# Kernel optimization log

Measured on AMD Instinct MI355X. Metric: run time of the kernel, lower is better.

The kernel has to match this reference:

```python
import jax, jax.numpy as jnp
import numpy as np

HD = 64        # hidden_dim
H = 4          # heads
N = 50000      # nodes
E = 400000     # edges (before self loops)
NEG_ATT = 0.2  # GATConv attention LeakyReLU slope (PyG default)
NEG_ACT = 0.01 # nn.LeakyReLU() default slope
EPS = 1e-5     # BatchNorm eps


def _bn(x, gamma, beta):
    # training-mode BatchNorm1d over node dimension (biased variance)
    mu = x.mean(0)
    var = x.var(0)
    return gamma * (x - mu) * jax.lax.rsqrt(var + EPS) + beta


def _gatconv(h_in, src, dst, W, a_src, a_dst, bias, heads, outc, concat):
    n = h_in.shape[0]
    h = (h_in @ W.T).reshape(n, heads, outc)              # [N,H,C]
    al_s = jnp.einsum('nhc,hc->nh', h, a_src)             # [N,H]
    al_d = jnp.einsum('nhc,hc->nh', h, a_dst)
    e = jax.nn.leaky_relu(al_s[src] + al_d[dst], NEG_ATT) # [E',H]
    # softmax over incoming edges of each destination node
    m = jax.lax.stop_gradient(jax.ops.segment_max(e, dst, num_segments=n))
    ex = jnp.exp(e - m[dst])
    den = jax.ops.segment_sum(ex, dst, num_segments=n)
    alpha = ex / den[dst]                                  # [E',H]
    out = jax.ops.segment_sum(h[src] * alpha[..., None], dst, num_segments=n)
    out = out.reshape(n, heads * outc) if concat else out.mean(axis=1)
    return out + bias


def setup_inputs() -> dict:
    ks = jax.random.split(jax.random.key(0), 20)
    s = 0.1
    d = {
        'x': jax.random.normal(ks[0], (N, 2 * HD), jnp.float32),
        'edge_index': jax.random.randint(ks[1], (2, E), 0, N, jnp.int64),
        'W1': jax.random.normal(ks[2], (H * HD, 2 * HD), jnp.float32) * s,
        'a1s': jax.random.normal(ks[3], (H, HD), jnp.float32) * s,
        'a1d': jax.random.normal(ks[4], (H, HD), jnp.float32) * s,
        'b1': jnp.zeros((H * HD,), jnp.float32),
        'W2': jax.random.normal(ks[5], (H * HD, H * HD), jnp.float32) * s,
        'a2s': jax.random.normal(ks[6], (H, HD), jnp.float32) * s,
        'a2d': jax.random.normal(ks[7], (H, HD), jnp.float32) * s,
        'b2': jnp.zeros((H * HD,), jnp.float32),
        'W3': jax.random.normal(ks[8], (1 * HD, H * HD), jnp.float32) * s,
        'a3s': jax.random.normal(ks[9], (1, HD), jnp.float32) * s,
        'a3d': jax.random.normal(ks[10], (1, HD), jnp.float32) * s,
        'b3': jnp.zeros((HD,), jnp.float32),
        'gamma': jnp.ones((H * HD,), jnp.float32),
        'beta': jnp.zeros((H * HD,), jnp.float32),
    }
    return d


def reference(x, edge_index, W1, a1s, a1d, b1, W2, a2s, a2d, b2,
              W3, a3s, a3d, b3, gamma, beta):
    n = x.shape[0]
    loop = jnp.arange(n, dtype=edge_index.dtype)
    src = jnp.concatenate([edge_index[0], loop])  # add_self_loops=True
    dst = jnp.concatenate([edge_index[1], loop])

    h = _gatconv(x, src, dst, W1, a1s, a1d, b1, H, HD, True)
    h = jax.nn.leaky_relu(_bn(h, gamma, beta), NEG_ACT)

    # single middle residual block (num_layers=3); dropout is identity (eval)
    res = h
    h = _gatconv(h, src, dst, W2, a2s, a2d, b2, H, HD, True)
    h = jax.nn.leaky_relu(_bn(h, gamma, beta), NEG_ACT)
    h = h + res

    out = _gatconv(h, src, dst, W3, a3s, a3d, b3, 1, HD, False)
    return out
```

## Files before the change

kernel.cpp:

```cpp
#include <hip/hip_runtime.h>
#include <hip/hip_bf16.h>

#define NEG_ATT 0.2f
#define NEG_ACT 0.01f

typedef __attribute__((ext_vector_type(8))) short short8;
typedef __attribute__((ext_vector_type(4))) float f32x4;

__device__ __forceinline__ unsigned short f2bf(float f) {
    unsigned int u = __float_as_uint(f);
    unsigned int r = (u + 0x7fff + ((u >> 16) & 1)) >> 16;
    return (unsigned short)r;
}
__device__ __forceinline__ float b2f(unsigned short h) {
    return __uint_as_float((unsigned int)h << 16);
}


__global__ void count_edges(const int* __restrict__ ei, int* deg, int E) {
    int t = blockIdx.x * 256 + threadIdx.x;
    if (t < E) atomicAdd(&deg[ei[E + t]], 1);
}

#define SCAN_CHUNK 1024
__global__ void scan1(const int* __restrict__ deg, int* __restrict__ offs,
                      int* blocksum, int Nn) {
    __shared__ int sh[256];
    int b = blockIdx.x, t = threadIdx.x;
    int base = b * SCAN_CHUNK + t * 4;
    int v[4];
    int s = 0;
    for (int j = 0; j < 4; j++) {
        int idx = base + j;
        v[j] = (idx < Nn) ? deg[idx] : 0;
        s += v[j];
    }
    sh[t] = s;
    __syncthreads();
    for (int off = 1; off < 256; off <<= 1) {
        int x = (t >= off) ? sh[t - off] : 0;
        __syncthreads();
        sh[t] += x;
        __syncthreads();
    }
    int excl = sh[t] - s;
    if (t == 255) blocksum[b] = sh[255];
    int run = excl;
    for (int j = 0; j < 4; j++) {
        int idx = base + j;
        if (idx < Nn) offs[idx] = run;
        run += v[j];
    }
}

__global__ void scan23(int* __restrict__ offs, const int* __restrict__ bsum,
                       int* __restrict__ cursor, int Nn, int G) {
    int i = blockIdx.x * 256 + threadIdx.x;
    if (i > Nn) return;
    int g = i >> 10;
    int basev = 0;
    for (int k = 0; k < g; k++) basev += bsum[k];
    if (i == Nn) {
        int tot = basev;
        for (int k = g; k < G; k++) tot += bsum[k];
        offs[Nn] = tot;
        return;
    }
    int v = offs[i] + basev;
    offs[i] = v;
    cursor[i] = v;
}

__global__ void fill_csr(const int* __restrict__ ei, int* cursor, int* csr, int E, int Nn) {
    int t = blockIdx.x * 256 + threadIdx.x;
    if (t < E) {
        int s = ei[t];
        int d = ei[E + t];
        int p = atomicAdd(&cursor[d], 1);
        csr[p] = s;
    } else if (t < E + Nn) {
        int nn = t - E;
        int p = atomicAdd(&cursor[nn], 1);
        csr[p] = nn;
    }
}


__global__ __launch_bounds__(256) void prep_all(
    int* __restrict__ deg, int Nn,
    const float* __restrict__ x, unsigned short* __restrict__ xb, int nx, int nxpad,
    const float* __restrict__ w1, unsigned short* __restrict__ o1, int n1,
    const float* __restrict__ w2, unsigned short* __restrict__ o2, int n2,
    const float* __restrict__ w3, unsigned short* __restrict__ o3, int n3) {
    int id = blockIdx.x * 256 + threadIdx.x;
    int nconv = (nxpad + n1 + n2 + n3) / 8;
    if (id >= nconv) {
        int d0 = (id - nconv) * 8;
        for (int k = 0; k < 8; k++)
            if (d0 + k < Nn) deg[d0 + k] = 1;
        return;
    }
    int i = id * 8;
    const float* in;
    unsigned short* out;
    if (i < nxpad) {
        if (i >= nx) {
            *(ushort4*)&xb[i] = make_ushort4(0, 0, 0, 0);
            *(ushort4*)&xb[i + 4] = make_ushort4(0, 0, 0, 0);
            return;
        }
        in = x + i; out = xb + i;
    } else {
        int j = i - nxpad;
        if (j < n1) { in = w1 + j; out = o1 + j; }
        else if (j < n1 + n2) { in = w2 + (j - n1); out = o2 + (j - n1); }
        else { in = w3 + (j - n1 - n2); out = o3 + (j - n1 - n2); }
    }
    float4 a = *(const float4*)in;
    float4 b = *(const float4*)(in + 4);
    *(ushort4*)out = make_ushort4(f2bf(a.x), f2bf(a.y), f2bf(a.z), f2bf(a.w));
    *(ushort4*)(out + 4) = make_ushort4(f2bf(b.x), f2bf(b.y), f2bf(b.z), f2bf(b.w));
}


template <int K, int CO, int HEADS>
__global__ __launch_bounds__(256) void gemm_mfma(
    const unsigned short* __restrict__ Xb, const unsigned short* __restrict__ Wb,
    unsigned short* __restrict__ Hb, const float* __restrict__ a_s,
    const float* __restrict__ a_d, float* __restrict__ als, float* __restrict__ ald) {
    constexpr int BM = 128, BN = 64, BK = 64, LD = 72, SLD = 68;
    __shared__ __align__(16) char smem[4 * 32 * SLD * 4];
    unsigned short* As = (unsigned short*)smem;
    unsigned short* Bs = As + BM * LD;
    int tid = threadIdx.x;
    int wave = tid >> 6, lane = tid & 63;
    int quad = lane >> 4, l16 = lane & 15;
    int m0 = blockIdx.x * BM, n0 = blockIdx.y * BN;
    int hd = blockIdx.y;
    int arow = tid >> 3;
    int achk = (tid & 7) * 8;
    f32x4 acc[2][4] = {};
    for (int k0 = 0; k0 < K; k0 += BK) {
        __syncthreads();
#pragma unroll
        for (int p = 0; p < 4; p++) {
            int r = arow + p * 32;
            *(int4*)&As[r * LD + achk] = *(const int4*)&Xb[(size_t)(m0 + r) * K + k0 + achk];
        }
#pragma unroll
        for (int p = 0; p < 2; p++) {
            int r = arow + p * 32;
            *(int4*)&Bs[r * LD + achk] = *(const int4*)&Wb[(size_t)(n0 + r) * K + k0 + achk];
        }
        __syncthreads();
#pragma unroll
        for (int ks = 0; ks < 2; ks++) {
            short8 af[2], bfr[4];
#pragma unroll
            for (int i = 0; i < 2; i++)
                af[i] = *(const short8*)&As[(wave * 32 + i * 16 + l16) * LD + ks * 32 + quad * 8];
#pragma unroll
            for (int j = 0; j < 4; j++)
                bfr[j] = *(const short8*)&Bs[(j * 16 + l16) * LD + ks * 32 + quad * 8];
#pragma unroll
            for (int i = 0; i < 2; i++)
#pragma unroll
                for (int j = 0; j < 4; j++)
                    acc[i][j] = __builtin_amdgcn_mfma_f32_16x16x32_bf16(af[i], bfr[j], acc[i][j], 0, 0, 0);
        }
    }
    __syncthreads();

    float asv[4], adv[4];
#pragma unroll
    for (int j = 0; j < 4; j++) {
        asv[j] = a_s[hd * 64 + j * 16 + l16];
        adv[j] = a_d[hd * 64 + j * 16 + l16];
    }
#pragma unroll
    for (int i = 0; i < 2; i++)
#pragma unroll
        for (int r = 0; r < 4; r++) {
            float ps = acc[i][0][r] * asv[0] + acc[i][1][r] * asv[1] +
                       acc[i][2][r] * asv[2] + acc[i][3][r] * asv[3];
            float pd = acc[i][0][r] * adv[0] + acc[i][1][r] * adv[1] +
                       acc[i][2][r] * adv[2] + acc[i][3][r] * adv[3];
#pragma unroll
            for (int mm = 1; mm < 16; mm <<= 1) {
                ps += __shfl_xor(ps, mm);
                pd += __shfl_xor(pd, mm);
            }
            if (l16 == 0) {
                int m = m0 + wave * 32 + i * 16 + quad * 4 + r;
                als[m * HEADS + hd] = ps;
                ald[m * HEADS + hd] = pd;
            }
        }

    float* stg = (float*)smem + wave * 32 * SLD;
#pragma unroll
    for (int i = 0; i < 2; i++)
#pragma unroll
        for (int j = 0; j < 4; j++)
#pragma unroll
            for (int r = 0; r < 4; r++)
                stg[(i * 16 + quad * 4 + r) * SLD + j * 16 + l16] = acc[i][j][r];
    int g = lane >> 3, c8 = (lane & 7) * 8;
#pragma unroll
    for (int p = 0; p < 4; p++) {
        int row = p * 8 + g;
        float4 v0 = *(const float4*)&stg[row * SLD + c8];
        float4 v1 = *(const float4*)&stg[row * SLD + c8 + 4];
        uint4 o;
        o.x = ((unsigned)f2bf(v0.y) << 16) | f2bf(v0.x);
        o.y = ((unsigned)f2bf(v0.w) << 16) | f2bf(v0.z);
        o.z = ((unsigned)f2bf(v1.y) << 16) | f2bf(v1.x);
        o.w = ((unsigned)f2bf(v1.w) << 16) | f2bf(v1.z);
        *(uint4*)&Hb[(size_t)(m0 + wave * 32 + row) * CO + n0 + c8] = o;
    }
}


#define EDGE4(sA, sB, sC, sD)                                                        \
    {                                                                                \
        float a0 = als[(sA)*4 + hd], a1 = als[(sB)*4 + hd];                          \
        float a2 = als[(sC)*4 + hd], a3 = als[(sD)*4 + hd];                          \
        ushort4 h0 = *(const ushort4*)&Hb[(size_t)(sA)*256 + c4];                    \
        ushort4 h1 = *(const ushort4*)&Hb[(size_t)(sB)*256 + c4];                    \
        ushort4 h2 = *(const ushort4*)&Hb[(size_t)(sC)*256 + c4];                    \
        ushort4 h3 = *(const ushort4*)&Hb[(size_t)(sD)*256 + c4];                    \
        float e0 = a0 + aldn; e0 = e0 > 0.f ? e0 : NEG_ATT * e0;                     \
        float e1 = a1 + aldn; e1 = e1 > 0.f ? e1 : NEG_ATT * e1;                     \
        float e2 = a2 + aldn; e2 = e2 > 0.f ? e2 : NEG_ATT * e2;                     \
        float e3 = a3 + aldn; e3 = e3 > 0.f ? e3 : NEG_ATT * e3;                     \
        float w0 = __expf(e0), w1 = __expf(e1), w2 = __expf(e2), w3 = __expf(e3);    \
        den += (w0 + w1) + (w2 + w3);                                                \
        acc.x += w0 * b2f(h0.x) + w1 * b2f(h1.x) + w2 * b2f(h2.x) + w3 * b2f(h3.x);  \
        acc.y += w0 * b2f(h0.y) + w1 * b2f(h1.y) + w2 * b2f(h2.y) + w3 * b2f(h3.y);  \
        acc.z += w0 * b2f(h0.z) + w1 * b2f(h1.z) + w2 * b2f(h2.z) + w3 * b2f(h3.z);  \
        acc.w += w0 * b2f(h0.w) + w1 * b2f(h1.w) + w2 * b2f(h2.w) + w3 * b2f(h3.w);  \
    }

__global__ __launch_bounds__(256) void aggregate_h4(
    const unsigned short* __restrict__ Hb, const float* __restrict__ als,
    const float* __restrict__ ald, const int* __restrict__ offs,
    const int* __restrict__ csr, unsigned short* __restrict__ Yb, int Nn) {
    int wave = threadIdx.x >> 6;
    int lane = threadIdx.x & 63;
    int n = blockIdx.x * 4 + wave;
    if (n >= Nn) return;
    int hd = lane >> 4;
    int c4 = lane * 4;
    float aldn = ald[n * 4 + hd];
    int beg = offs[n], end = offs[n + 1];
    float4 acc = make_float4(0.f, 0.f, 0.f, 0.f);
    float den = 0.f;
    for (int b = beg; b < end; b += 64) {
        int cnt = min(64, end - b);
        int idx = 0;
        if (lane < cnt) idx = csr[b + lane];
        int j = 0;
        for (; j + 8 <= cnt; j += 8) {
            int s0 = __shfl(idx, j), s1 = __shfl(idx, j + 1);
            int s2 = __shfl(idx, j + 2), s3 = __shfl(idx, j + 3);
            int s4 = __shfl(idx, j + 4), s5 = __shfl(idx, j + 5);
            int s6 = __shfl(idx, j + 6), s7 = __shfl(idx, j + 7);
            EDGE4(s0, s1, s2, s3);
            EDGE4(s4, s5, s6, s7);
        }
        for (; j + 4 <= cnt; j += 4) {
            int s0 = __shfl(idx, j), s1 = __shfl(idx, j + 1);
            int s2 = __shfl(idx, j + 2), s3 = __shfl(idx, j + 3);
            EDGE4(s0, s1, s2, s3);
        }
        for (; j < cnt; j++) {
            int s = __shfl(idx, j);
            float e = als[s * 4 + hd] + aldn;
            e = e > 0.f ? e : NEG_ATT * e;
            float w = __expf(e);
            den += w;
            ushort4 hv = *(const ushort4*)&Hb[(size_t)s * 256 + c4];
            acc.x += w * b2f(hv.x); acc.y += w * b2f(hv.y);
            acc.z += w * b2f(hv.z); acc.w += w * b2f(hv.w);
        }
    }
    float inv = 1.f / den;
    *(ushort4*)&Yb[(size_t)n * 256 + c4] = make_ushort4(
        f2bf(acc.x * inv), f2bf(acc.y * inv), f2bf(acc.z * inv), f2bf(acc.w * inv));
}

__global__ __launch_bounds__(256) void aggregate_h1(
    const unsigned short* __restrict__ Hb, const float* __restrict__ als,
    const float* __restrict__ ald, const int* __restrict__ offs,
    const int* __restrict__ csr, const float* __restrict__ bias,
    float* __restrict__ Yout, int Nn) {
    int wave = threadIdx.x >> 6;
    int lane = threadIdx.x & 63;
    int sub = lane >> 4, lane16 = lane & 15;
    int n = blockIdx.x * 16 + wave * 4 + sub;
    if (n >= Nn) return;
    int c4 = lane16 * 4;
    float aldn = ald[n];
    int beg = offs[n], end = offs[n + 1];
    float4 acc = make_float4(0.f, 0.f, 0.f, 0.f);
    float den = 0.f;
    for (int b = beg; b < end; b += 16) {
        int cnt = min(16, end - b);
        int idx = 0;
        if (lane16 < cnt) idx = csr[b + lane16];
        int j = 0;
        for (; j + 4 <= cnt; j += 4) {
            int s0 = __shfl(idx, (sub << 4) + j);
            int s1 = __shfl(idx, (sub << 4) + j + 1);
            int s2 = __shfl(idx, (sub << 4) + j + 2);
            int s3 = __shfl(idx, (sub << 4) + j + 3);
            float a0 = als[s0], a1 = als[s1], a2 = als[s2], a3 = als[s3];
            ushort4 h0 = *(const ushort4*)&Hb[(size_t)s0 * 64 + c4];
            ushort4 h1 = *(const ushort4*)&Hb[(size_t)s1 * 64 + c4];
            ushort4 h2 = *(const ushort4*)&Hb[(size_t)s2 * 64 + c4];
            ushort4 h3 = *(const ushort4*)&Hb[(size_t)s3 * 64 + c4];
            float e0 = a0 + aldn; e0 = e0 > 0.f ? e0 : NEG_ATT * e0;
            float e1 = a1 + aldn; e1 = e1 > 0.f ? e1 : NEG_ATT * e1;
            float e2 = a2 + aldn; e2 = e2 > 0.f ? e2 : NEG_ATT * e2;
            float e3 = a3 + aldn; e3 = e3 > 0.f ? e3 : NEG_ATT * e3;
            float w0 = __expf(e0), w1 = __expf(e1), w2 = __expf(e2), w3 = __expf(e3);
            den += (w0 + w1) + (w2 + w3);
            acc.x += w0 * b2f(h0.x) + w1 * b2f(h1.x) + w2 * b2f(h2.x) + w3 * b2f(h3.x);
            acc.y += w0 * b2f(h0.y) + w1 * b2f(h1.y) + w2 * b2f(h2.y) + w3 * b2f(h3.y);
            acc.z += w0 * b2f(h0.z) + w1 * b2f(h1.z) + w2 * b2f(h2.z) + w3 * b2f(h3.z);
            acc.w += w0 * b2f(h0.w) + w1 * b2f(h1.w) + w2 * b2f(h2.w) + w3 * b2f(h3.w);
        }
        for (; j < cnt; j++) {
            int s = __shfl(idx, (sub << 4) + j);
            float e = als[s] + aldn;
            e = e > 0.f ? e : NEG_ATT * e;
            float w = __expf(e);
            den += w;
            ushort4 hv = *(const ushort4*)&Hb[(size_t)s * 64 + c4];
            acc.x += w * b2f(hv.x); acc.y += w * b2f(hv.y);
            acc.z += w * b2f(hv.z); acc.w += w * b2f(hv.w);
        }
    }
    float inv = 1.f / den;
    float4 bv = *(const float4*)&bias[c4];
    float4 o = make_float4(acc.x * inv + bv.x, acc.y * inv + bv.y,
                           acc.z * inv + bv.z, acc.w * inv + bv.w);
    *(float4*)&Yout[(size_t)n * 64 + c4] = o;
}


__global__ __launch_bounds__(256) void bn_stats(const unsigned short* __restrict__ Yb,
                                                float* __restrict__ partial, int Nn) {
    __shared__ float red[4 * 512];
    int t = threadIdx.x;
    int g = blockIdx.x;
    int rows_per = (Nn + gridDim.x - 1) / gridDim.x;
    int r0 = g * rows_per;
    int r1 = min(r0 + rows_per, Nn);
    int sub = t >> 6;
    int c4 = (t & 63) * 4;
    float4 s = make_float4(0.f, 0.f, 0.f, 0.f);
    float4 q = make_float4(0.f, 0.f, 0.f, 0.f);
    for (int r = r0 + sub; r < r1; r += 4) {
        ushort4 u = *(const ushort4*)&Yb[(size_t)r * 256 + c4];
        float vx = b2f(u.x), vy = b2f(u.y), vz = b2f(u.z), vw = b2f(u.w);
        s.x += vx; s.y += vy; s.z += vz; s.w += vw;
        q.x += vx * vx; q.y += vy * vy; q.z += vz * vz; q.w += vw * vw;
    }
    float* rs = &red[sub * 512];
    rs[c4 + 0] = s.x; rs[c4 + 1] = s.y; rs[c4 + 2] = s.z; rs[c4 + 3] = s.w;
    rs[256 + c4 + 0] = q.x; rs[256 + c4 + 1] = q.y;
    rs[256 + c4 + 2] = q.z; rs[256 + c4 + 3] = q.w;
    __syncthreads();
    float v0 = red[t] + red[512 + t] + red[1024 + t] + red[1536 + t];
    float v1 = red[256 + t] + red[768 + t] + red[1280 + t] + red[1792 + t];
    partial[(size_t)g * 512 + t] = v0;
    partial[(size_t)g * 512 + 256 + t] = v1;
}

__global__ __launch_bounds__(256) void bn_reduce_final(
    const float* __restrict__ partial, int NP, const float* __restrict__ gamma,
    const float* __restrict__ beta, float* scale, float* shift, int Nn) {
    __shared__ float sh[8];
    int ch = blockIdx.x;
    int t = threadIdx.x;
    int wave = t >> 6, lane = t & 63;
    float s = 0.f, q = 0.f;
    for (int i = t; i < NP; i += 256) {
        s += partial[(size_t)i * 512 + ch];
        q += partial[(size_t)i * 512 + 256 + ch];
    }
    for (int off = 32; off; off >>= 1) {
        s += __shfl_down(s, off);
        q += __shfl_down(q, off);
    }
    if (lane == 0) { sh[wave] = s; sh[4 + wave] = q; }
    __syncthreads();
    if (t == 0) {
        s = sh[0] + sh[1] + sh[2] + sh[3];
        q = sh[4] + sh[5] + sh[6] + sh[7];
        float inv_n = 1.f / (float)Nn;
        float mu = s * inv_n;
        float var = q * inv_n - mu * mu;
        float sc = gamma[ch] * rsqrtf(var + 1e-5f);
        scale[ch] = sc;
        shift[ch] = beta[ch] - mu * sc;
    }
}

template <bool RES>
__global__ __launch_bounds__(256) void bn_apply(const unsigned short* __restrict__ Yb,
                                                const float* __restrict__ scale,
                                                const float* __restrict__ shift,
                                                unsigned short* __restrict__ OutB,
                                                int total4, int total4pad) {
    int i = blockIdx.x * 256 + threadIdx.x;
    if (i >= total4pad) return;
    if (i >= total4) {
        *(ushort4*)&OutB[i * 4] = make_ushort4(0, 0, 0, 0);
        return;
    }
    ushort4 u = *(const ushort4*)&Yb[i * 4];
    int cb = (i * 4) & 255;
    float4 sc = *(const float4*)&scale[cb];
    float4 sh = *(const float4*)&shift[cb];
    float4 o;
    o.x = sc.x * b2f(u.x) + sh.x; o.x = o.x > 0.f ? o.x : NEG_ACT * o.x;
    o.y = sc.y * b2f(u.y) + sh.y; o.y = o.y > 0.f ? o.y : NEG_ACT * o.y;
    o.z = sc.z * b2f(u.z) + sh.z; o.z = o.z > 0.f ? o.z : NEG_ACT * o.z;
    o.w = sc.w * b2f(u.w) + sh.w; o.w = o.w > 0.f ? o.w : NEG_ACT * o.w;
    if (RES) {
        ushort4 r = *(const ushort4*)&OutB[i * 4];
        o.x += b2f(r.x); o.y += b2f(r.y); o.z += b2f(r.z); o.w += b2f(r.w);
    }
    *(ushort4*)&OutB[i * 4] = make_ushort4(f2bf(o.x), f2bf(o.y), f2bf(o.z), f2bf(o.w));
}


extern "C" void kernel_launch(void* const* d_in, const int* in_sizes, int n_in,
                              void* d_out, int out_size, void* d_ws, size_t ws_size,
                              hipStream_t stream) {
    const float* x    = (const float*)d_in[0];
    const int*   ei   = (const int*)d_in[1];
    const float* W1   = (const float*)d_in[2];
    const float* a1s  = (const float*)d_in[3];
    const float* a1d  = (const float*)d_in[4];
    const float* W2   = (const float*)d_in[6];
    const float* a2s  = (const float*)d_in[7];
    const float* a2d  = (const float*)d_in[8];
    const float* W3   = (const float*)d_in[10];
    const float* a3s  = (const float*)d_in[11];
    const float* a3d  = (const float*)d_in[12];
    const float* b3   = (const float*)d_in[13];
    const float* gamma = (const float*)d_in[14];
    const float* beta  = (const float*)d_in[15];
    float* out = (float*)d_out;

    const int Nn = in_sizes[0] / 128;
    const int E  = in_sizes[1] / 2;
    const int Ep = E + Nn;
    const int Mpad = (Nn + 127) & ~127;

    size_t off = 0;
    char* base = (char*)d_ws;
    auto alloc = [&](size_t bytes) -> void* {
        void* p = base + off;
        off = (off + bytes + 255) & ~(size_t)255;
        return p;
    };
    unsigned short* Hb   = (unsigned short*)alloc((size_t)Mpad * 256 * 2);
    unsigned short* Yb   = (unsigned short*)alloc((size_t)Nn * 256 * 2);
    unsigned short* xb1  = (unsigned short*)alloc((size_t)Mpad * 128 * 2);
    unsigned short* xbig = (unsigned short*)alloc((size_t)Mpad * 256 * 2);
    unsigned short* wb1  = (unsigned short*)alloc((size_t)256 * 128 * 2);
    unsigned short* wb2  = (unsigned short*)alloc((size_t)256 * 256 * 2);
    unsigned short* wb3  = (unsigned short*)alloc((size_t)64 * 256 * 2);
    float* als    = (float*)alloc((size_t)Mpad * 4 * 4);
    float* ald    = (float*)alloc((size_t)Mpad * 4 * 4);
    int*   deg    = (int*)alloc((size_t)Nn * 4);
    int*   offs   = (int*)alloc((size_t)(Nn + 1) * 4);
    int*   cursor = (int*)alloc((size_t)Nn * 4);
    int*   bsum   = (int*)alloc(64 * 4);
    int*   csr    = (int*)alloc((size_t)Ep * 4);
    const int NP = 1024;
    float* partial = (float*)alloc((size_t)NP * 512 * 4);
    float* scale  = (float*)alloc(256 * 4);
    float* shift  = (float*)alloc(256 * 4);
    (void)ws_size;

    const int G = (Nn + SCAN_CHUNK - 1) / SCAN_CHUNK;

    {
        int nxpad = Mpad * 128;
        int wtot = 256 * 128 + 256 * 256 + 64 * 256;
        int nconv = (nxpad + wtot) / 8;
        int ndeg = (Nn + 7) / 8;
        prep_all<<<(nconv + ndeg + 255) / 256, 256, 0, stream>>>(
            deg, Nn, x, xb1, Nn * 128, nxpad,
            W1, wb1, 256 * 128, W2, wb2, 256 * 256, W3, wb3, 64 * 256);
    }

    count_edges<<<(E + 255) / 256, 256, 0, stream>>>(ei, deg, E);
    scan1<<<G, 256, 0, stream>>>(deg, offs, bsum, Nn);
    scan23<<<(Nn + 1 + 255) / 256, 256, 0, stream>>>(offs, bsum, cursor, Nn, G);
    fill_csr<<<(Ep + 255) / 256, 256, 0, stream>>>(ei, cursor, csr, E, Nn);

    const int gm = Mpad / 128;
    const int nagg4 = (Nn + 3) / 4;
    const int nagg1 = (Nn + 15) / 16;
    const int total4 = Nn * 64;
    const int total4pad = Mpad * 64;
    const int napply = (total4pad + 255) / 256;

    gemm_mfma<128, 256, 4><<<dim3(gm, 4), 256, 0, stream>>>(xb1, wb1, Hb, a1s, a1d, als, ald);
    aggregate_h4<<<nagg4, 256, 0, stream>>>(Hb, als, ald, offs, csr, Yb, Nn);
    bn_stats<<<NP, 256, 0, stream>>>(Yb, partial, Nn);
    bn_reduce_final<<<256, 256, 0, stream>>>(partial, NP, gamma, beta, scale, shift, Nn);
    bn_apply<false><<<napply, 256, 0, stream>>>(Yb, scale, shift, xbig, total4, total4pad);

    gemm_mfma<256, 256, 4><<<dim3(gm, 4), 256, 0, stream>>>(xbig, wb2, Hb, a2s, a2d, als, ald);
    aggregate_h4<<<nagg4, 256, 0, stream>>>(Hb, als, ald, offs, csr, Yb, Nn);
    bn_stats<<<NP, 256, 0, stream>>>(Yb, partial, Nn);
    bn_reduce_final<<<256, 256, 0, stream>>>(partial, NP, gamma, beta, scale, shift, Nn);
    bn_apply<true><<<napply, 256, 0, stream>>>(Yb, scale, shift, xbig, total4, total4pad);

    gemm_mfma<256, 64, 1><<<dim3(gm, 1), 256, 0, stream>>>(xbig, wb3, Hb, a3s, a3d, als, ald);
    aggregate_h1<<<nagg1, 256, 0, stream>>>(Hb, als, ald, offs, csr, b3, out, Nn);
}
```

Baseline: 339.5 us.

## Compute all heads per GEMM block and fold edge counting into prep kernel

Adds a gemm_wide kernel where each block computes all 256 output columns (four heads), so each X tile is loaded once rather than once per head-block. The attention logits for all heads are reduced in the epilogue. Separately, degree counting moves into the prep_all kernel after a memset, with the self-loop +1 applied in the scan, removing a launch. The wide tile needs many accumulator registers and gives fewer blocks, which may lower occupancy and parallelism.

```diff
diff --git a/kernel.cpp b/kernel.cpp
--- a/kernel.cpp
+++ b/kernel.cpp
@@ -16,11 +16,6 @@
     return __uint_as_float((unsigned int)h << 16);
 }
 
-
-__global__ void count_edges(const int* __restrict__ ei, int* deg, int E) {
-    int t = blockIdx.x * 256 + threadIdx.x;
-    if (t < E) atomicAdd(&deg[ei[E + t]], 1);
-}
 
 #define SCAN_CHUNK 1024
 __global__ void scan1(const int* __restrict__ deg, int* __restrict__ offs,
@@ -32,7 +27,7 @@
     int s = 0;
     for (int j = 0; j < 4; j++) {
         int idx = base + j;
-        v[j] = (idx < Nn) ? deg[idx] : 0;
+        v[j] = (idx < Nn) ? deg[idx] + 1 : 0;
         s += v[j];
     }
     sh[t] = s;
@@ -87,7 +82,7 @@
 
 
 __global__ __launch_bounds__(256) void prep_all(
-    int* __restrict__ deg, int Nn,
+    int* __restrict__ deg, const int* __restrict__ ei, int E,
     const float* __restrict__ x, unsigned short* __restrict__ xb, int nx, int nxpad,
     const float* __restrict__ w1, unsigned short* __restrict__ o1, int n1,
     const float* __restrict__ w2, unsigned short* __restrict__ o2, int n2,
@@ -95,9 +90,8 @@
     int id = blockIdx.x * 256 + threadIdx.x;
     int nconv = (nxpad + n1 + n2 + n3) / 8;
     if (id >= nconv) {
-        int d0 = (id - nconv) * 8;
-        for (int k = 0; k < 8; k++)
-            if (d0 + k < Nn) deg[d0 + k] = 1;
+        int e = id - nconv;
+        if (e < E) atomicAdd(&deg[ei[E + e]], 1);
         return;
     }
     int i = id * 8;
@@ -123,19 +117,121 @@
 }
 
 
+template <int K>
+__global__ __launch_bounds__(256) void gemm_wide(
+    const unsigned short* __restrict__ Xb, const unsigned short* __restrict__ Wb,
+    unsigned short* __restrict__ Hb, const float* __restrict__ a_s,
+    const float* __restrict__ a_d, float* __restrict__ als, float* __restrict__ ald) {
+    constexpr int BM = 128, BK = 64, LD = 72, SLD = 68;
+    __shared__ __align__(16) char smem[(BM + 256) * LD * 2];
+    unsigned short* As = (unsigned short*)smem;
+    unsigned short* Bs = As + BM * LD;
+    int tid = threadIdx.x;
+    int wave = tid >> 6, lane = tid & 63;
+    int quad = lane >> 4, l16 = lane & 15;
+    int m0 = blockIdx.x * BM;
+    int arow = tid >> 3;
+    int achk = (tid & 7) * 8;
+    f32x4 acc[2][16] = {};
+    for (int k0 = 0; k0 < K; k0 += BK) {
+        __syncthreads();
+#pragma unroll
+        for (int p = 0; p < 4; p++) {
+            int r = arow + p * 32;
+            *(int4*)&As[r * LD + achk] = *(const int4*)&Xb[(size_t)(m0 + r) * K + k0 + achk];
+        }
+#pragma unroll
+        for (int p = 0; p < 8; p++) {
+            int r = arow + p * 32;
+            *(int4*)&Bs[r * LD + achk] = *(const int4*)&Wb[(size_t)r * K + k0 + achk];
+        }
+        __syncthreads();
+#pragma unroll
+        for (int ks = 0; ks < 2; ks++) {
+            short8 af[2];
+#pragma unroll
+            for (int i = 0; i < 2; i++)
+                af[i] = *(const short8*)&As[(wave * 32 + i * 16 + l16) * LD + ks * 32 + quad * 8];
+#pragma unroll
+            for (int j = 0; j < 16; j++) {
+                short8 bfr = *(const short8*)&Bs[(j * 16 + l16) * LD + ks * 32 + quad * 8];
+                acc[0][j] = __builtin_amdgcn_mfma_f32_16x16x32_bf16(af[0], bfr, acc[0][j], 0, 0, 0);
+                acc[1][j] = __builtin_amdgcn_mfma_f32_16x16x32_bf16(af[1], bfr, acc[1][j], 0, 0, 0);
+            }
+        }
+    }
+    __syncthreads();
+
+#pragma unroll
+    for (int hd = 0; hd < 4; hd++) {
+        float asv[4], adv[4];
+#pragma unroll
+        for (int j = 0; j < 4; j++) {
+            asv[j] = a_s[hd * 64 + j * 16 + l16];
+            adv[j] = a_d[hd * 64 + j * 16 + l16];
+        }
+#pragma unroll
+        for (int i = 0; i < 2; i++)
+#pragma unroll
+            for (int r = 0; r < 4; r++) {
+                float ps = acc[i][hd * 4 + 0][r] * asv[0] + acc[i][hd * 4 + 1][r] * asv[1] +
+                           acc[i][hd * 4 + 2][r] * asv[2] + acc[i][hd * 4 + 3][r] * asv[3];
+                float pd = acc[i][hd * 4 + 0][r] * adv[0] + acc[i][hd * 4 + 1][r] * adv[1] +
+                           acc[i][hd * 4 + 2][r] * adv[2] + acc[i][hd * 4 + 3][r] * adv[3];
+#pragma unroll
+                for (int mm = 1; mm < 16; mm <<= 1) {
+                    ps += __shfl_xor(ps, mm);
+                    pd += __shfl_xor(pd, mm);
+                }
+                if (l16 == 0) {
+                    int m = m0 + wave * 32 + i * 16 + quad * 4 + r;
+                    als[m * 4 + hd] = ps;
+                    ald[m * 4 + hd] = pd;
+                }
+            }
+    }
+
+    float* stg = (float*)smem + wave * 32 * SLD;
+    int g = lane >> 3, c8 = (lane & 7) * 8;
+#pragma unroll
+    for (int hd = 0; hd < 4; hd++) {
+#pragma unroll
+        for (int i = 0; i < 2; i++)
+#pragma unroll
+            for (int j = 0; j < 4; j++)
+#pragma unroll
+                for (int r = 0; r < 4; r++)
+                    stg[(i * 16 + quad * 4 + r) * SLD + j * 16 + l16] = acc[i][hd * 4 + j][r];
+        __builtin_amdgcn_s_waitcnt(0);
+#pragma unroll
+        for (int p = 0; p < 4; p++) {
+            int row = p * 8 + g;
+            float4 v0 = *(const float4*)&stg[row * SLD + c8];
+            float4 v1 = *(const float4*)&stg[row * SLD + c8 + 4];
+            uint4 o;
+            o.x = ((unsigned)f2bf(v0.y) << 16) | f2bf(v0.x);
+            o.y = ((unsigned)f2bf(v0.w) << 16) | f2bf(v0.z);
+            o.z = ((unsigned)f2bf(v1.y) << 16) | f2bf(v1.x);
+            o.w = ((unsigned)f2bf(v1.w) << 16) | f2bf(v1.z);
+            *(uint4*)&Hb[(size_t)(m0 + wave * 32 + row) * 256 + hd * 64 + c8] = o;
+        }
+    }
+}
+
+
 template <int K, int CO, int HEADS>
 __global__ __launch_bounds__(256) void gemm_mfma(
     const unsigned short* __restrict__ Xb, const unsigned short* __restrict__ Wb,
     unsigned short* __restrict__ Hb, const float* __restrict__ a_s,
     const float* __restrict__ a_d, float* __restrict__ als, float* __restrict__ ald) {
-    constexpr int BM = 128, BN = 64, BK = 64, LD = 72, SLD = 68;
+    constexpr int BM = 128, BK = 64, LD = 72, SLD = 68;
     __shared__ __align__(16) char smem[4 * 32 * SLD * 4];
     unsigned short* As = (unsigned short*)smem;
     unsigned short* Bs = As + BM * LD;
     int tid = threadIdx.x;
     int wave = tid >> 6, lane = tid & 63;
     int quad = lane >> 4, l16 = lane & 15;
-    int m0 = blockIdx.x * BM, n0 = blockIdx.y * BN;
+    int m0 = blockIdx.x * BM, n0 = blockIdx.y * 64;
     int hd = blockIdx.y;
     int arow = tid >> 3;
     int achk = (tid & 7) * 8;
@@ -490,17 +586,16 @@
 
     const int G = (Nn + SCAN_CHUNK - 1) / SCAN_CHUNK;
 
+    hipMemsetAsync(deg, 0, (size_t)Nn * 4, stream);
     {
         int nxpad = Mpad * 128;
         int wtot = 256 * 128 + 256 * 256 + 64 * 256;
         int nconv = (nxpad + wtot) / 8;
-        int ndeg = (Nn + 7) / 8;
-        prep_all<<<(nconv + ndeg + 255) / 256, 256, 0, stream>>>(
-            deg, Nn, x, xb1, Nn * 128, nxpad,
+        prep_all<<<(nconv + E + 255) / 256, 256, 0, stream>>>(
+            deg, ei, E, x, xb1, Nn * 128, nxpad,
             W1, wb1, 256 * 128, W2, wb2, 256 * 256, W3, wb3, 64 * 256);
     }
 
-    count_edges<<<(E + 255) / 256, 256, 0, stream>>>(ei, deg, E);
     scan1<<<G, 256, 0, stream>>>(deg, offs, bsum, Nn);
     scan23<<<(Nn + 1 + 255) / 256, 256, 0, stream>>>(offs, bsum, cursor, Nn, G);
     fill_csr<<<(Ep + 255) / 256, 256, 0, stream>>>(ei, cursor, csr, E, Nn);
@@ -512,13 +607,13 @@
     const int total4pad = Mpad * 64;
     const int napply = (total4pad + 255) / 256;
 
-    gemm_mfma<128, 256, 4><<<dim3(gm, 4), 256, 0, stream>>>(xb1, wb1, Hb, a1s, a1d, als, ald);
+    gemm_wide<128><<<gm, 256, 0, stream>>>(xb1, wb1, Hb, a1s, a1d, als, ald);
     aggregate_h4<<<nagg4, 256, 0, stream>>>(Hb, als, ald, offs, csr, Yb, Nn);
     bn_stats<<<NP, 256, 0, stream>>>(Yb, partial, Nn);
     bn_reduce_final<<<256, 256, 0, stream>>>(partial, NP, gamma, beta, scale, shift, Nn);
     bn_apply<false><<<napply, 256, 0, stream>>>(Yb, scale, shift, xbig, total4, total4pad);
 
-    gemm_mfma<256, 256, 4><<<dim3(gm, 4), 256, 0, stream>>>(xbig, wb2, Hb, a2s, a2d, als, ald);
+    gemm_wide<256><<<gm, 256, 0, stream>>>(xbig, wb2, Hb, a2s, a2d, als, ald);
     aggregate_h4<<<nagg4, 256, 0, stream>>>(Hb, als, ald, offs, csr, Yb, Nn);
     bn_stats<<<NP, 256, 0, stream>>>(Yb, partial, Nn);
     bn_reduce_final<<<256, 256, 0, stream>>>(partial, NP, gamma, beta, scale, shift, Nn);
```

Result: slower. 353.1 us (+4.0%).
